# Kernel tuning notes

Hardware: AMD Instinct MI355X
Metric: run time of the kernel (lower is better)

The kernel has to match this reference:

```python
import jax, jax.numpy as jnp
import numpy as np

TEMPERATURE = 2.0
FACTOR = 0.8
NEG = 256
EPS = 1e-8  # torch CosineSimilarity eps


def setup_inputs() -> dict:
    key = jax.random.key(0)
    ks = jax.random.split(key, 5)
    B, C, H, W = 4, 64, 64, 64
    views_1 = jax.random.normal(ks[0], (B, C, H, W), jnp.float32)
    views_2 = jax.random.normal(ks[1], (B, C, H, W), jnp.float32)
    img = jax.random.uniform(ks[2], (1, 3, H, W), dtype=jnp.float32)
    neg_idx_h = jax.random.randint(ks[3], (B, H * W, NEG), 0, H, dtype=jnp.int32)
    neg_idx_w = jax.random.randint(ks[4], (B, H * W, NEG), 0, W, dtype=jnp.int32)
    return {"views_1": views_1, "views_2": views_2, "img": img,
            "neg_idx_h": neg_idx_h, "neg_idx_w": neg_idx_w}


def reference(views_1, views_2, img, neg_idx_h, neg_idx_w):
    B, C, H, W = views_1.shape
    HW = H * W
    hh = (jnp.arange(HW) // W).astype(jnp.float32)   # pixel row coords [HW]
    ww = (jnp.arange(HW) % W).astype(jnp.float32)    # pixel col coords [HW]
    max_euc = jnp.sqrt(jnp.asarray((H - 1) ** 2 + (W - 1) ** 2, jnp.float32))
    max_rgb = jnp.sqrt(jnp.asarray(3.0, jnp.float32))
    img0 = img[0].reshape(3, HW)                     # [3,HW] (original always uses img[0])

    def per_item(z1, z2, ih, iw):
        z1v = z1.reshape(C, HW)                      # [C,HW] anchor patches
        pn = z2[:, ih, iw]                           # [C,HW,NEG] gathered negatives
        n1 = jnp.sqrt(jnp.sum(z1v * z1v, axis=0))    # [HW]
        n2 = jnp.sqrt(jnp.sum(pn * pn, axis=0))      # [HW,NEG]
        dot = jnp.einsum('cp,cpk->pk', z1v, pn)      # [HW,NEG]
        cos_neg = dot / jnp.maximum(n1[:, None] * n2, EPS)
        cos_self = (n1 * n1) / jnp.maximum(n1 * n1, EPS)   # ~1 per pixel
        ihf = ih.astype(jnp.float32)
        iwf = iw.astype(jnp.float32)
        euc = jnp.sqrt((hh[:, None] - ihf) ** 2 + (ww[:, None] - iwf) ** 2) / max_euc
        img_neg = img[0][:, ih, iw]                  # [3,HW,NEG]
        rgb = jnp.sqrt(jnp.sum((img0[:, :, None] - img_neg) ** 2, axis=0)) / max_rgb
        weight = euc * FACTOR + rgb * (1.0 - FACTOR)
        sim_neg = jnp.minimum(jnp.abs(cos_neg * weight), 1.0)   # abs then clamp at 1
        sim_self = jnp.minimum(jnp.abs(cos_self), 1.0)
        s0 = jnp.sum(sim_self) / HW                  # positive sim (scalar)
        sneg = jnp.sum(sim_neg, axis=0) / HW / TEMPERATURE     # [NEG]
        sim_vec = jnp.concatenate([s0[None], sneg])  # [NEG+1]
        # BCE with target=[1,0,...,0]; torch BCE clamps log at -100
        log_s0 = jnp.maximum(jnp.log(s0), -100.0)
        log_1m = jnp.maximum(jnp.log(1.0 - sneg), -100.0)
        bce = -(log_s0 + jnp.sum(log_1m)) / (NEG + 1)
        return bce, sim_vec

    bce, sim_vecs = jax.vmap(per_item)(views_1, views_2, neg_idx_h, neg_idx_w)
    sim_all = jnp.sum(sim_vecs, axis=0)              # [NEG+1]
    loss = jnp.mean(bce)
    return (loss,
            sim_all[0] / B,
            sim_all[1:].sum() / NEG * TEMPERATURE / B)
```

## Files before the change

### kernel.cpp

```cpp
#include <hip/hip_runtime.h>
#include <math.h>

typedef unsigned short ushort;
typedef unsigned int uint;
typedef unsigned char uchar;

#define B 4
#define C 64
#define H 64
#define W 64
#define HW 4096
#define NEG 256
#define NGRP 16
#define PXB 64
#define NBLK (B * HW / PXB)

#define QS 7.49f
#define INVQS2 (1.0f / (QS * QS))
#define RGBNORM5 0.0186243f

#define OFF_Z2A    0
#define OFF_Z2B    (OFF_Z2A + B*HW*4)
#define OFF_N1MAP  (OFF_Z2B + B*HW*4)
#define OFF_IMGU16 (OFF_N1MAP + B*HW)
#define OFF_PART2  (OFF_IMGU16 + HW/2)

__device__ __forceinline__ int nib(uint u, int j) {
    return ((int)(u << (28 - 4 * j))) >> 28;
}
__device__ __forceinline__ int dot8(uint a, uint b, int c) {
#if __has_builtin(__builtin_amdgcn_sdot8)
    return __builtin_amdgcn_sdot8((int)a, (int)b, c, false);
#else
#pragma unroll
    for (int j = 0; j < 8; ++j) c += nib(a, j) * nib(b, j);
    return c;
#endif
}

__global__ __launch_bounds__(256) void k_prep(const float* __restrict__ v2,
                                              const float* __restrict__ v1,
                                              const float* __restrict__ img,
                                              uchar* __restrict__ z2Ag,
                                              uchar* __restrict__ z2Bg,
                                              float* __restrict__ n1map,
                                              ushort* __restrict__ img_u16,
                                              float* __restrict__ partial2) {
    int t = threadIdx.x;
    if (blockIdx.x < 256) {
        __shared__ float tile[64][65];
        __shared__ float npart[4][64];
        __shared__ float ninv[64];
        int b  = blockIdx.x >> 6;
        int q0 = (blockIdx.x & 63) * 64;
        int qq = t & 63;
        int cg = t >> 6;
        const float* src = v2 + (size_t)b * C * HW;
        float acc = 0.f;
#pragma unroll
        for (int r = 0; r < 16; ++r) {
            int c = cg * 16 + r;
            float v = src[(size_t)c * HW + q0 + qq];
            tile[c][qq] = v;
            acc += v * v;
        }
        npart[cg][qq] = acc;
        __syncthreads();
        if (t < 64) {
            float s = npart[0][t] + npart[1][t] + npart[2][t] + npart[3][t];
            ninv[t] = QS / fmaxf(sqrtf(s), 1e-8f);
        }
        __syncthreads();
        int qw   = t >> 2;
        int quad = t & 3;
        int c0   = quad * 16;
        float inv = ninv[qw];
        uint u0 = 0, u1 = 0;
#pragma unroll
        for (int j = 0; j < 8; ++j) {
            int x0 = (int)rintf(tile[c0 + j][qw] * inv);
            int x1 = (int)rintf(tile[c0 + 8 + j][qw] * inv);
            u0 |= (uint)(x0 & 0xF) << (4 * j);
            u1 |= (uint)(x1 & 0xF) << (4 * j);
        }
        size_t col = (size_t)b * HW + q0 + qw;
        uint2 val = make_uint2(u0, u1);
        if (quad < 2) *(uint2*)(z2Ag + col * 16 + quad * 8)       = val;
        else          *(uint2*)(z2Bg + col * 16 + (quad - 2) * 8) = val;
    } else {
        int bid = blockIdx.x - 256;
        int b = bid >> 4;
        int q = (bid & 15) * 256 + t;
        partial2[bid * 256 + t] = 0.f;
        const float* src = v1 + (size_t)b * C * HW + q;
        float acc = 0.f;
#pragma unroll 8
        for (int c = 0; c < C; ++c) {
            float v = src[(size_t)c * HW];
            acc += v * v;
        }
        n1map[b * HW + q] = sqrtf(acc);
        if (b == 0) {
            uint r  = (uint)rintf(img[q] * 31.f);
            uint g  = (uint)rintf(img[HW + q] * 31.f);
            uint bl = (uint)rintf(img[2 * HW + q] * 31.f);
            img_u16[q] = (ushort)(r | (g << 5) | (bl << 10));
        }
    }
}

__global__ __launch_bounds__(1024) void k_main(const float* __restrict__ v1,
                                               const int* __restrict__ negh,
                                               const int* __restrict__ negw,
                                               const uint4* __restrict__ z2Ag,
                                               const uint4* __restrict__ z2Bg,
                                               const float* __restrict__ n1map,
                                               const ushort* __restrict__ img_u16,
                                               float* __restrict__ partial2) {
    __shared__ uint4 zA[HW];
    __shared__ uint4 zB[HW];
    __shared__ ushort imgu[HW];
    __shared__ uint z1q[PXB][8];
    int b  = blockIdx.x >> 6;
    int p0 = (blockIdx.x & 63) * PXB;
    int t  = threadIdx.x;

    {
        const uint4* gA = z2Ag + (size_t)b * HW;
        const uint4* gB = z2Bg + (size_t)b * HW;
#pragma unroll
        for (int i = 0; i < 4; ++i) {
            zA[i * 1024 + t] = gA[i * 1024 + t];
            zB[i * 1024 + t] = gB[i * 1024 + t];
        }
        if (t < 512) ((uint4*)imgu)[t] = ((const uint4*)img_u16)[t];
    }
    if (t < 512) {
        int px = t >> 3;
        int ui = t & 7;
        const float* srcb = v1 + (size_t)b * C * HW + p0 + px;
        float inv = QS / fmaxf(n1map[b * HW + p0 + px], 1e-8f);
        uint u = 0;
#pragma unroll
        for (int j = 0; j < 8; ++j) {
            int x = (int)rintf(srcb[(size_t)(8 * ui + j) * HW] * inv);
            u |= (uint)(x & 0xF) << (4 * j);
        }
        z1q[px][ui] = u;
    }
    __syncthreads();

    const float inv_max_euc = 1.0f / sqrtf((float)((H - 1) * (H - 1) + (W - 1) * (W - 1)));
    int k       = t & 255;
    int quarter = t >> 8;
    int pbase   = p0 + quarter * 16;
    const int* nh = negh + ((size_t)b * HW + pbase) * NEG + k;
    const int* nw = negw + ((size_t)b * HW + pbase) * NEG + k;

    float acc = 0.f;
#pragma unroll 2
    for (int j0 = 0; j0 < 16; j0 += 8) {
        int ihv[8], iwv[8];
#pragma unroll
        for (int j = 0; j < 8; ++j) {
            ihv[j] = nh[(j0 + j) * NEG];
            iwv[j] = nw[(j0 + j) * NEG];
        }
#pragma unroll
        for (int j = 0; j < 8; ++j) {
            int px = quarter * 16 + j0 + j;
            int p  = pbase + j0 + j;
            int ih = ihv[j], iw = iwv[j];
            int qv = (ih << 6) + iw;
            float dh = (float)(p >> 6) - (float)ih;
            float dw = (float)(p & 63) - (float)iw;
            float euc = sqrtf(dh * dh + dw * dw) * inv_max_euc;
            uint up = imgu[p];
            uint uq = imgu[qv];
            int dr = (int)(up & 31u)         - (int)(uq & 31u);
            int dg = (int)((up >> 5) & 31u)  - (int)((uq >> 5) & 31u);
            int db = (int)((up >> 10) & 31u) - (int)((uq >> 10) & 31u);
            float rgb = sqrtf((float)(dr * dr + dg * dg + db * db)) * RGBNORM5;
            float wv = (0.8f * euc + 0.2f * rgb) * INVQS2;
            uint4 A  = zA[qv];
            uint4 Bv = zB[qv];
            const uint4* zc = (const uint4*)(&z1q[px][0]);
            uint4 u0 = zc[0];
            uint4 u1 = zc[1];
            int di = 0;
            di = dot8(A.x,  u0.x, di);
            di = dot8(A.y,  u0.y, di);
            di = dot8(A.z,  u0.z, di);
            di = dot8(A.w,  u0.w, di);
            di = dot8(Bv.x, u1.x, di);
            di = dot8(Bv.y, u1.y, di);
            di = dot8(Bv.z, u1.z, di);
            di = dot8(Bv.w, u1.w, di);
            acc += fminf(fabsf((float)di * wv), 1.0f);
        }
    }
    atomicAdd(&partial2[((size_t)b * NGRP + ((blockIdx.x & 63) >> 2)) * NEG + k], acc);
}

__global__ __launch_bounds__(256) void k_reduce2f(const float* __restrict__ partial2,
                                                  const float* __restrict__ n1map,
                                                  float* __restrict__ out) {
    __shared__ float xw[3][4];
    int t = threadIdx.x;
    int lane = t & 63;
    int wid  = t >> 6;
    float bsum = 0.f, s0sum = 0.f, snegsum = 0.f;
    for (int b = 0; b < B; ++b) {
        float s = 0.f;
#pragma unroll
        for (int g = 0; g < NGRP; ++g)
            s += partial2[((size_t)b * NGRP + g) * NEG + t];
        float sneg = s * (1.0f / HW) * 0.5f;
        float l1m  = fmaxf(logf(1.0f - sneg), -100.0f);
        float ss = 0.f;
#pragma unroll
        for (int j = 0; j < HW / 256; ++j) {
            float n1 = n1map[b * HW + j * 256 + t];
            float n1sq = n1 * n1;
            ss += fminf(n1sq / fmaxf(n1sq, 1e-8f), 1.0f);
        }
        float r0 = sneg, r1 = l1m, r2 = ss;
#pragma unroll
        for (int o = 1; o < 64; o <<= 1) {
            r0 += __shfl_xor(r0, o);
            r1 += __shfl_xor(r1, o);
            r2 += __shfl_xor(r2, o);
        }
        if (lane == 0) { xw[0][wid] = r0; xw[1][wid] = r1; xw[2][wid] = r2; }
        __syncthreads();
        if (t == 0) {
            float sn = xw[0][0] + xw[0][1] + xw[0][2] + xw[0][3];
            float lm = xw[1][0] + xw[1][1] + xw[1][2] + xw[1][3];
            float sv = xw[2][0] + xw[2][1] + xw[2][2] + xw[2][3];
            float s0 = sv * (1.0f / HW);
            bsum    += -(fmaxf(logf(s0), -100.0f) + lm) * (1.0f / (NEG + 1));
            s0sum   += s0;
            snegsum += sn;
        }
        __syncthreads();
    }
    if (t == 0) {
        out[0] = bsum * 0.25f;
        out[1] = s0sum * 0.25f;
        out[2] = snegsum * (1.0f / NEG) * 2.0f * 0.25f;
    }
}

extern "C" void kernel_launch(void* const* d_in, const int* in_sizes, int n_in,
                              void* d_out, int out_size, void* d_ws, size_t ws_size,
                              hipStream_t stream) {
    const float* v1   = (const float*)d_in[0];
    const float* v2   = (const float*)d_in[1];
    const float* img  = (const float*)d_in[2];
    const int*   negh = (const int*)d_in[3];
    const int*   negw = (const int*)d_in[4];
    float* out = (float*)d_out;
    float* ws  = (float*)d_ws;

    uchar*  z2Ag     = (uchar*)(ws + OFF_Z2A);
    uchar*  z2Bg     = (uchar*)(ws + OFF_Z2B);
    float*  n1map    = ws + OFF_N1MAP;
    ushort* img_u16  = (ushort*)(ws + OFF_IMGU16);
    float*  partial2 = ws + OFF_PART2;

    hipLaunchKernelGGL(k_prep, dim3(320), dim3(256), 0, stream,
                       v2, v1, img, z2Ag, z2Bg, n1map, img_u16, partial2);
    hipLaunchKernelGGL(k_main, dim3(NBLK), dim3(1024), 0, stream,
                       v1, negh, negw, (const uint4*)z2Ag, (const uint4*)z2Bg,
                       n1map, img_u16, partial2);
    hipLaunchKernelGGL(k_reduce2f, dim3(1), dim3(256), 0, stream, partial2, n1map, out);
}
```

Measured before the change: 32.77 us.

## Batch LDS gathers ahead of dot products and reduce atomics in shared memory

Splits the inner loop into phases. Weights and indices are computed first, then all eight zA/zB rows are gathered from LDS, then the dot8 products run, so the LDS loads are issued together and their latency overlaps. The outer loop is fully unrolled and the launch bounds gain an occupancy hint. The four quarter-warps' partial sums are combined in a shared array before one global atomic per negative, which cuts global atomics fourfold. In exchange it adds a barrier and more register pressure.

```diff
diff --git a/kernel.cpp b/kernel.cpp
--- a/kernel.cpp
+++ b/kernel.cpp
@@ -109,18 +109,19 @@
     }
 }
 
-__global__ __launch_bounds__(1024) void k_main(const float* __restrict__ v1,
-                                               const int* __restrict__ negh,
-                                               const int* __restrict__ negw,
-                                               const uint4* __restrict__ z2Ag,
-                                               const uint4* __restrict__ z2Bg,
-                                               const float* __restrict__ n1map,
-                                               const ushort* __restrict__ img_u16,
-                                               float* __restrict__ partial2) {
+__global__ __launch_bounds__(1024, 4) void k_main(const float* __restrict__ v1,
+                                                  const int* __restrict__ negh,
+                                                  const int* __restrict__ negw,
+                                                  const uint4* __restrict__ z2Ag,
+                                                  const uint4* __restrict__ z2Bg,
+                                                  const float* __restrict__ n1map,
+                                                  const ushort* __restrict__ img_u16,
+                                                  float* __restrict__ partial2) {
     __shared__ uint4 zA[HW];
     __shared__ uint4 zB[HW];
     __shared__ ushort imgu[HW];
     __shared__ uint z1q[PXB][8];
+    __shared__ float redk[NEG];
     int b  = blockIdx.x >> 6;
     int p0 = (blockIdx.x & 63) * PXB;
     int t  = threadIdx.x;
@@ -134,6 +135,7 @@
             zB[i * 1024 + t] = gB[i * 1024 + t];
         }
         if (t < 512) ((uint4*)imgu)[t] = ((const uint4*)img_u16)[t];
+        if (t < NEG) redk[t] = 0.f;
     }
     if (t < 512) {
         int px = t >> 3;
@@ -158,7 +160,7 @@
     const int* nw = negw + ((size_t)b * HW + pbase) * NEG + k;
 
     float acc = 0.f;
-#pragma unroll 2
+#pragma unroll
     for (int j0 = 0; j0 < 16; j0 += 8) {
         int ihv[8], iwv[8];
 #pragma unroll
@@ -166,9 +168,10 @@
             ihv[j] = nh[(j0 + j) * NEG];
             iwv[j] = nw[(j0 + j) * NEG];
         }
-#pragma unroll
-        for (int j = 0; j < 8; ++j) {
-            int px = quarter * 16 + j0 + j;
+        int   qvv[8];
+        float wvv[8];
+#pragma unroll
+        for (int j = 0; j < 8; ++j) {
             int p  = pbase + j0 + j;
             int ih = ihv[j], iw = iwv[j];
             int qv = (ih << 6) + iw;
@@ -181,25 +184,38 @@
             int dg = (int)((up >> 5) & 31u)  - (int)((uq >> 5) & 31u);
             int db = (int)((up >> 10) & 31u) - (int)((uq >> 10) & 31u);
             float rgb = sqrtf((float)(dr * dr + dg * dg + db * db)) * RGBNORM5;
-            float wv = (0.8f * euc + 0.2f * rgb) * INVQS2;
-            uint4 A  = zA[qv];
-            uint4 Bv = zB[qv];
+            wvv[j] = (0.8f * euc + 0.2f * rgb) * INVQS2;
+            qvv[j] = qv;
+        }
+        uint4 Av[8], Bv[8];
+#pragma unroll
+        for (int j = 0; j < 8; ++j) {
+            Av[j] = zA[qvv[j]];
+            Bv[j] = zB[qvv[j]];
+        }
+#pragma unroll
+        for (int j = 0; j < 8; ++j) {
+            int px = quarter * 16 + j0 + j;
             const uint4* zc = (const uint4*)(&z1q[px][0]);
             uint4 u0 = zc[0];
             uint4 u1 = zc[1];
             int di = 0;
-            di = dot8(A.x,  u0.x, di);
-            di = dot8(A.y,  u0.y, di);
-            di = dot8(A.z,  u0.z, di);
-            di = dot8(A.w,  u0.w, di);
-            di = dot8(Bv.x, u1.x, di);
-            di = dot8(Bv.y, u1.y, di);
-            di = dot8(Bv.z, u1.z, di);
-            di = dot8(Bv.w, u1.w, di);
-            acc += fminf(fabsf((float)di * wv), 1.0f);
-        }
-    }
-    atomicAdd(&partial2[((size_t)b * NGRP + ((blockIdx.x & 63) >> 2)) * NEG + k], acc);
+            di = dot8(Av[j].x, u0.x, di);
+            di = dot8(Av[j].y, u0.y, di);
+            di = dot8(Av[j].z, u0.z, di);
+            di = dot8(Av[j].w, u0.w, di);
+            di = dot8(Bv[j].x, u1.x, di);
+            di = dot8(Bv[j].y, u1.y, di);
+            di = dot8(Bv[j].z, u1.z, di);
+            di = dot8(Bv[j].w, u1.w, di);
+            acc += fminf(fabsf((float)di * wvv[j]), 1.0f);
+        }
+    }
+    atomicAdd(&redk[k], acc);
+    __syncthreads();
+    if (t < NEG)
+        atomicAdd(&partial2[((size_t)b * NGRP + ((blockIdx.x & 63) >> 2)) * NEG + t],
+                  redk[t]);
 }
 
 __global__ __launch_bounds__(256) void k_reduce2f(const float* __restrict__ partial2,
```

Measured after the change: 34.27 us. 4.6% more time.
